# Kernel tuning notes

Measured on AMD Instinct MI355X. Metric: run time of the kernel, lower is better.

The kernel has to match this reference:

```python
import jax, jax.numpy as jnp
import numpy as np

NX = 65536      # x_steps_soil
T_STEPS = 200   # t_steps
HID = 32        # function_learner hidden width


def setup_inputs() -> dict:
    key = jax.random.key(0)
    ks = jax.random.split(key, 6)
    # u0: stacked (c, sk) initial state, values in [0, 1)
    u0 = jax.random.uniform(ks[0], (NX, 2), dtype=jnp.float32)
    t = jnp.arange(T_STEPS, dtype=jnp.float32)  # uniform time grid, dt = 1

    def lin(k, fan_in, fan_out):
        W = jax.random.normal(k, (fan_in, fan_out), dtype=jnp.float32) / np.float32(np.sqrt(fan_in))
        b = jnp.zeros((fan_out,), dtype=jnp.float32)
        return W, b

    # func_r: [1 -> 32 -> 32 -> 32 -> 1], tanh hidden, sigmoid output (sigmoid=True)
    W0, b0 = lin(ks[1], 1, HID)
    W1, b1 = lin(ks[2], HID, HID)
    W2, b2 = lin(ks[3], HID, HID)
    W3, b3 = lin(ks[4], HID, 1)

    return dict(
        u0=u0, t=t,
        W0=W0, b0=b0, W1=W1, b1=b1, W2=W2, b2=b2, W3=W3, b3=b3,
        ret_fac=jnp.float32(1.0),            # self.ret_fac
        D=jnp.float32(1e-5),                 # diffusion coefficient
        stencil=jnp.array([-1.0, 1.0], dtype=jnp.float32),
        BC=jnp.float32(1.0),                 # top Dirichlet BC value
        f=jnp.float32(0.5),                  # kinetic/instantaneous sorption share
        k_d=jnp.float32(1.0),                # Freundlich constant
        beta=jnp.float32(0.8),               # Freundlich exponent
        alpha=jnp.float32(0.05),             # kinetic rate constant
        rho_s=jnp.float32(1.5),              # bulk density
        n_e=jnp.float32(0.3),                # porosity
        v_e=jnp.float32(0.005),              # effective velocity
        dx=jnp.float32(0.01),                # spatial step
    )


def reference(u0, t, W0, b0, W1, b1, W2, b2, W3, b3,
              ret_fac, D, stencil, BC, f, k_d, beta, alpha, rho_s, n_e, v_e, dx):
    dt = t[1] - t[0]

    def mlp_r(c):
        # per-cell learned retardation multiplier (func_r), sigmoid output in (0,1)
        h = jnp.tanh(c[:, None] @ W0 + b0)   # [Nx, H]
        h = jnp.tanh(h @ W1 + b1)
        h = jnp.tanh(h @ W2 + b2)
        return jax.nn.sigmoid(h @ W3 + b3)[:, 0]  # [Nx]

    def rhs(u):
        c, sk = u[:, 0], u[:, 1]
        ret = mlp_r(c) * ret_fac
        # neighbor values: Dirichlet BC at top, zero-gradient at bottom
        cl = jnp.concatenate([jnp.full((1,), BC, dtype=c.dtype), c[:-1]])
        cr = jnp.concatenate([c[1:], c[-1:]])
        # stencil fluxes (stencil = [-1, 1])
        lf = stencil[0] * c + stencil[1] * cl
        lf = lf.at[0].multiply(2.0)  # half-cell distance at Dirichlet boundary
        rf = stencil[0] * c + stencil[1] * cr  # rf[-1] == 0: no-flux bottom
        diff = D / dx**2 * (lf + rf)
        # upwind advection (flow from top to bottom)
        adv = v_e / dx * (c - cl)
        # two-site sorption kinetics (Freundlich isotherm)
        dsk = alpha * ((1.0 - f) * k_d * jnp.power(jnp.clip(c, 1e-9, None), beta) - sk)
        dc = ret * (diff - adv) - (rho_s / n_e) * dsk
        return jnp.stack([dc, dsk], axis=-1)  # [Nx, 2]

    def step(u, _):
        u2 = u + dt * rhs(u)
        return u2, u2

    _, traj = jax.lax.scan(step, u0, None, length=t.shape[0])
    return traj  # [T, Nx, 2]
```

## Files before the change

kernel.cpp:

```cpp
#include <hip/hip_runtime.h>
#include <stdint.h>

#define NXS    65536
#define HID    32
#define BTL    512
#define NB     256
#define OWNB   256
#define MARG   200
#define SSPAN  656
#define SLAB   128
#define EPOCH  24
#define LUT_N  1024
#define NREP   16
#define LUT_SC   512.0f
#define LUT_BF   128.0f

typedef float    f32x4 __attribute__((ext_vector_type(4)));
typedef uint32_t u32x4 __attribute__((ext_vector_type(4)));

__device__ __forceinline__ float fexp2(float x) { return __builtin_amdgcn_exp2f(x); }
__device__ __forceinline__ float frcp(float x)  { return __builtin_amdgcn_rcpf(x); }
__device__ __forceinline__ float flog2(float x) { return __builtin_amdgcn_logf(x); }

__device__ __forceinline__ float dpp_up(float x) {
    int xi = __float_as_int(x);
    return __int_as_float(__builtin_amdgcn_update_dpp(xi, xi, 0x138, 0xF, 0xF, false));
}
__device__ __forceinline__ float dpp_down(float x) {
    int xi = __float_as_int(x);
    return __int_as_float(__builtin_amdgcn_update_dpp(xi, xi, 0x130, 0xF, 0xF, false));
}

__device__ __forceinline__ float fast_tanh(float x) {
    x = fminf(fmaxf(x, -15.0f), 15.0f);
    float e = fexp2(x * 2.8853900817779268f);
    return (e - 1.0f) * frcp(e + 1.0f);
}
__device__ __forceinline__ float fast_sigmoid(float x) {
    float e = fexp2(x * -1.4426950408889634f);
    return frcp(1.0f + e);
}

struct FinnPtrs {
    const float* tvec;
    const float* Dp;  const float* stencil; const float* BCp; const float* fp;
    const float* kdp; const float* betap;   const float* alphap; const float* rhosp;
    const float* nep; const float* vep;     const float* dxp;
};

__global__ __launch_bounds__(256) void finn_lut(
    const float* __restrict__ W0, const float* __restrict__ b0,
    const float* __restrict__ W1, const float* __restrict__ b1,
    const float* __restrict__ W2, const float* __restrict__ b2,
    const float* __restrict__ W3, const float* __restrict__ b3,
    const float* __restrict__ ret_fac, const float* __restrict__ betap,
    float2* __restrict__ rep)
{
    const int i = blockIdx.x * 256 + threadIdx.x;
    if (i >= LUT_N) return;
    const float c = -0.25f + ((float)i + 0.5f) * (1.0f / LUT_SC);

    float h[HID], a[HID];
    #pragma unroll
    for (int j = 0; j < HID; ++j)
        h[j] = fast_tanh(fmaf(c, W0[j], b0[j]));

    #pragma unroll
    for (int j = 0; j < HID; ++j) a[j] = b1[j];
    #pragma unroll
    for (int k = 0; k < HID; ++k) {
        const float hk = h[k];
        #pragma unroll
        for (int j = 0; j < HID; ++j) a[j] = fmaf(hk, W1[k * HID + j], a[j]);
    }
    #pragma unroll
    for (int j = 0; j < HID; ++j) h[j] = fast_tanh(a[j]);

    #pragma unroll
    for (int j = 0; j < HID; ++j) a[j] = b2[j];
    #pragma unroll
    for (int k = 0; k < HID; ++k) {
        const float hk = h[k];
        #pragma unroll
        for (int j = 0; j < HID; ++j) a[j] = fmaf(hk, W2[k * HID + j], a[j]);
    }
    #pragma unroll
    for (int j = 0; j < HID; ++j) h[j] = fast_tanh(a[j]);

    float pre = b3[0];
    #pragma unroll
    for (int k = 0; k < HID; ++k) pre = fmaf(h[k], W3[k], pre);

    const float ret = fast_sigmoid(pre) * ret_fac[0];
    const float pw  = fexp2(betap[0] * flog2(fmaxf(c, 1e-9f)));
    const float2 e = make_float2(ret, pw);
    #pragma unroll
    for (int r = 0; r < NREP; ++r)
        rep[i * NREP + r] = e;
}

__global__ __launch_bounds__(BTL, 2) void finn_sweep(
    const float* __restrict__ uin, float* __restrict__ out,
    const float2* __restrict__ rep_g, FinnPtrs P, int T, uint32_t outBytes)
{
    __shared__ float2 slut[LUT_N * NREP];
    __shared__ float2 xbuf[SSPAN];

    const int tid  = threadIdx.x;
    const int w    = tid >> 6;
    const int lane = tid & 63;
    const int r15  = lane & 15;

    {
        const f32x4* src4 = (const f32x4*)rep_g;
        f32x4* dst4 = (f32x4*)slut;
        #pragma unroll
        for (int j = 0; j < (LUT_N * NREP * 8 / 16) / BTL; ++j)
            dst4[tid + j * BTL] = src4[tid + j * BTL];
    }

    const float dt   = P.tvec[1] - P.tvec[0];
    const float s0   = P.stencil[0];
    const float s1   = P.stencil[1];
    const float dx   = P.dxp[0];
    const float A    = P.Dp[0] / (dx * dx);
    const float B    = P.vep[0] / dx;
    const float BC   = P.BCp[0];
    const float alp  = P.alphap[0];
    const float akd  = (1.0f - P.fp[0]) * P.kdp[0];
    const float rsne = P.rhosp[0] / P.nep[0];

    const float G     = dt * rsne * alp;
    const float mGAKD = -G * akd;
    const float S1c   = 1.0f - dt * alp;
    const float S2c   = dt * alp * akd;
    const float K1u   = dt * (2.0f * A * s0 - B);
    const float K2u   = dt * (A * s1 + B);
    const float K3u   = dt * A * s1;

    const int b = blockIdx.x;
    int blockBase = b * OWNB - MARG;
    if (blockBase < 0) blockBase = 0;
    if (blockBase > NXS - SSPAN) blockBase = NXS - SSPAN;
    const bool leftA  = (blockBase == 0);
    const bool rightA = (blockBase == NXS - SSPAN);
    const int ownRelL = b * OWNB - blockBase;
    const int ownRelR = ownRelL + OWNB;

    u32x4 srd;
    {
        const uint64_t op = (uint64_t)(uintptr_t)out;
        srd.x = (uint32_t)op;
        srd.y = (uint32_t)(op >> 32);
        srd.z = outBytes;
        srd.w = 0x00020000u;
    }

    int a = ((SSPAN - SLAB) * w / 7 + 1) & ~1;

    float c0, sk0, c1, sk1;
    {
        const f32x4* u4 = (const f32x4*)uin;
        const f32x4 u = u4[(blockBase + a + lane * 2) >> 1];
        c0 = u.x; sk0 = u.y; c1 = u.z; sk1 = u.w;
    }

    __syncthreads();

    int done = 0;
    while (done < T) {
        int nst = T - done; if (nst > EPOCH) nst = EPOCH;
        const int si = a + lane * 2;
        const int g0 = blockBase + si;

        float K0_0 = 0.0f, K1_0 = K1u, K2_0 = K2u;
        const float K3_0 = K3u;
        float K1_1 = K1u, K3_1 = K3u;
        const float K2_1 = K2u;
        if (g0 == 0)           { K0_0 = dt * BC * (2.0f * A * s1 + B);
                                 K1_0 = dt * (3.0f * A * s0 - B); K2_0 = 0.0f; }
        if (g0 + 1 == NXS - 1) { K1_1 = dt * (2.0f * A * s0 - B + A * s1);
                                 K3_1 = 0.0f; }

        const int vL = leftA ? 0 : done;
        const int vR = rightA ? SSPAN : SSPAN - done;
        const int pd = vR - vL - SLAB;
        const int aPrev = vL + ((pd * (w - 1) / 7 + 1) & ~1);
        const int aNext = vL + ((pd * (w + 1) / 7 + 1) & ~1);
        int bLo = (w == 0) ? 0     : (((aPrev + SLAB + a) >> 1) & ~1);
        int bHi = (w == 7) ? SSPAN : (((a + SLAB + aNext) >> 1) & ~1);
        if (bLo < ownRelL) bLo = ownRelL;
        if (bHi > ownRelR) bHi = ownRelR;
        const bool st = (si >= bLo) && (si < bHi);
        uint32_t voff = st ? (uint32_t)((done * NXS + g0) * 8) : 0x60000000u;

        float clS = dpp_up(c1);
        float crS = dpp_down(c0);
        int i0 = (int)__builtin_amdgcn_fmed3f(fmaf(c0, LUT_SC, LUT_BF), 0.0f, 1023.0f);
        int i1 = (int)__builtin_amdgcn_fmed3f(fmaf(c1, LUT_SC, LUT_BF), 0.0f, 1023.0f);
        float2 E0 = slut[(i0 << 4) | r15];
        float2 E1 = slut[(i1 << 4) | r15];

        for (int s = 0; s < nst; ++s) {
            float t0 = fmaf(K1_0, c0, K0_0);
            t0 = fmaf(K2_0, clS, t0);
            t0 = fmaf(K3_0, c1, t0);
            float t1 = K1_1 * c1;
            t1 = fmaf(K2_1, c0, t1);
            t1 = fmaf(K3_1, crS, t1);

            float v0 = fmaf(E0.x, t0, c0); v0 = fmaf(mGAKD, E0.y, v0);
            float v1 = fmaf(E1.x, t1, c1); v1 = fmaf(mGAKD, E1.y, v1);
            const float nc0 = fmaf(G, sk0, v0);
            const float nc1 = fmaf(G, sk1, v1);
            sk0 = fmaf(S1c, sk0, S2c * E0.y);
            sk1 = fmaf(S1c, sk1, S2c * E1.y);
            c0 = nc0; c1 = nc1;

            i0 = (int)__builtin_amdgcn_fmed3f(fmaf(c0, LUT_SC, LUT_BF), 0.0f, 1023.0f);
            i1 = (int)__builtin_amdgcn_fmed3f(fmaf(c1, LUT_SC, LUT_BF), 0.0f, 1023.0f);
            E0 = slut[(i0 << 4) | r15];
            E1 = slut[(i1 << 4) | r15];
            clS = dpp_up(c1);
            crS = dpp_down(c0);

            f32x4 ov; ov.x = c0; ov.y = sk0; ov.z = c1; ov.w = sk1;
            asm volatile("buffer_store_dwordx4 %0, %1, %2, 0 offen"
                         :: "v"(ov), "v"(voff), "s"(srd) : "memory");
            voff += (uint32_t)(NXS * 8);
        }

        done += nst;
        if (done >= T) break;

        asm volatile("s_waitcnt lgkmcnt(0)" ::: "memory");
        __builtin_amdgcn_s_barrier();
        asm volatile("" ::: "memory");
        {
            const int wLo = (w == 0 && leftA)  ? 0    : EPOCH;
            const int wHi = (w == 7 && rightA) ? SLAB : SLAB - EPOCH;
            const int sr = lane * 2;
            if (sr >= wLo && sr < wHi)         xbuf[a + sr]     = make_float2(c0, sk0);
            if (sr + 1 >= wLo && sr + 1 < wHi) xbuf[a + sr + 1] = make_float2(c1, sk1);
        }
        asm volatile("s_waitcnt lgkmcnt(0)" ::: "memory");
        __builtin_amdgcn_s_barrier();
        asm volatile("" ::: "memory");
        {
            const int vL2 = leftA ? 0 : done;
            const int vR2 = rightA ? SSPAN : SSPAN - done;
            const int pd2 = vR2 - vL2 - SLAB;
            a = vL2 + ((pd2 * w / 7 + 1) & ~1);
            const f32x4 u = *(const f32x4*)&xbuf[a + lane * 2];
            c0 = u.x; sk0 = u.y; c1 = u.z; sk1 = u.w;
        }
        asm volatile("s_waitcnt lgkmcnt(0)" ::: "memory");
        __builtin_amdgcn_s_barrier();
        asm volatile("" ::: "memory");
    }
}

extern "C" void kernel_launch(void* const* d_in, const int* in_sizes, int n_in,
                              void* d_out, int out_size, void* d_ws, size_t ws_size,
                              hipStream_t stream)
{
    const float* u0 = (const float*)d_in[0];
    FinnPtrs P;
    P.tvec    = (const float*)d_in[1];
    const float* W0      = (const float*)d_in[2];
    const float* b0      = (const float*)d_in[3];
    const float* W1      = (const float*)d_in[4];
    const float* b1      = (const float*)d_in[5];
    const float* W2      = (const float*)d_in[6];
    const float* b2      = (const float*)d_in[7];
    const float* W3      = (const float*)d_in[8];
    const float* b3      = (const float*)d_in[9];
    const float* ret_fac = (const float*)d_in[10];
    P.Dp      = (const float*)d_in[11];
    P.stencil = (const float*)d_in[12];
    P.BCp     = (const float*)d_in[13];
    P.fp      = (const float*)d_in[14];
    P.kdp     = (const float*)d_in[15];
    P.betap   = (const float*)d_in[16];
    P.alphap  = (const float*)d_in[17];
    P.rhosp   = (const float*)d_in[18];
    P.nep     = (const float*)d_in[19];
    P.vep     = (const float*)d_in[20];
    P.dxp     = (const float*)d_in[21];

    float*  out = (float*)d_out;
    float2* rep = (float2*)d_ws;
    const int T = in_sizes[1];

    hipLaunchKernelGGL(finn_lut, dim3(LUT_N / 256), dim3(256), 0, stream,
                       W0, b0, W1, b1, W2, b2, W3, b3, ret_fac, P.betap, rep);

    hipLaunchKernelGGL(finn_sweep, dim3(NB), dim3(BTL), 0, stream,
                       u0, out, rep, P, T, (uint32_t)out_size * 4u);
}
```

Baseline: 62.65 us.

## Fuse LUT build into sweep kernel with linear interpolation and software-pipelined lookups

Drops the separate LUT kernel. Each block now evaluates the MLP on 1024 grid points itself, and stores slope/intercept pairs so the retardation is linearly interpolated instead of piecewise-constant. The Freundlich power is computed exactly with exp2/log2 per step rather than read from the table. After a safe number of steps, the LDS lookup for the next step is issued ahead of the arithmetic to hide latency. The trade-off is that every block repeats the MLP work, and each step does more transcendental math.

```diff
diff --git a/kernel.cpp b/kernel.cpp
--- a/kernel.cpp
+++ b/kernel.cpp
@@ -10,10 +10,11 @@
 #define SSPAN  656
 #define SLAB   128
 #define EPOCH  24
+#define SAFE_T 48
 #define LUT_N  1024
 #define NREP   16
-#define LUT_SC   512.0f
-#define LUT_BF   128.0f
+#define LUT_SC 512.0f
+#define LUT_BF 128.0f
 
 typedef float    f32x4 __attribute__((ext_vector_type(4)));
 typedef uint32_t u32x4 __attribute__((ext_vector_type(4)));
@@ -41,6 +42,11 @@
     return frcp(1.0f + e);
 }
 
+struct FinnW {
+    const float* W0; const float* b0; const float* W1; const float* b1;
+    const float* W2; const float* b2; const float* W3; const float* b3;
+    const float* ret_fac;
+};
 struct FinnPtrs {
     const float* tvec;
     const float* Dp;  const float* stencil; const float* BCp; const float* fp;
@@ -48,60 +54,40 @@
     const float* nep; const float* vep;     const float* dxp;
 };
 
-__global__ __launch_bounds__(256) void finn_lut(
-    const float* __restrict__ W0, const float* __restrict__ b0,
-    const float* __restrict__ W1, const float* __restrict__ b1,
-    const float* __restrict__ W2, const float* __restrict__ b2,
-    const float* __restrict__ W3, const float* __restrict__ b3,
-    const float* __restrict__ ret_fac, const float* __restrict__ betap,
-    float2* __restrict__ rep)
-{
-    const int i = blockIdx.x * 256 + threadIdx.x;
-    if (i >= LUT_N) return;
-    const float c = -0.25f + ((float)i + 0.5f) * (1.0f / LUT_SC);
-
+__device__ float mlp_ret(float c, const FinnW& W) {
     float h[HID], a[HID];
     #pragma unroll
     for (int j = 0; j < HID; ++j)
-        h[j] = fast_tanh(fmaf(c, W0[j], b0[j]));
-
-    #pragma unroll
-    for (int j = 0; j < HID; ++j) a[j] = b1[j];
+        h[j] = fast_tanh(fmaf(c, W.W0[j], W.b0[j]));
+    #pragma unroll
+    for (int j = 0; j < HID; ++j) a[j] = W.b1[j];
     #pragma unroll
     for (int k = 0; k < HID; ++k) {
         const float hk = h[k];
         #pragma unroll
-        for (int j = 0; j < HID; ++j) a[j] = fmaf(hk, W1[k * HID + j], a[j]);
+        for (int j = 0; j < HID; ++j) a[j] = fmaf(hk, W.W1[k * HID + j], a[j]);
     }
     #pragma unroll
     for (int j = 0; j < HID; ++j) h[j] = fast_tanh(a[j]);
-
-    #pragma unroll
-    for (int j = 0; j < HID; ++j) a[j] = b2[j];
+    #pragma unroll
+    for (int j = 0; j < HID; ++j) a[j] = W.b2[j];
     #pragma unroll
     for (int k = 0; k < HID; ++k) {
         const float hk = h[k];
         #pragma unroll
-        for (int j = 0; j < HID; ++j) a[j] = fmaf(hk, W2[k * HID + j], a[j]);
+        for (int j = 0; j < HID; ++j) a[j] = fmaf(hk, W.W2[k * HID + j], a[j]);
     }
     #pragma unroll
     for (int j = 0; j < HID; ++j) h[j] = fast_tanh(a[j]);
-
-    float pre = b3[0];
-    #pragma unroll
-    for (int k = 0; k < HID; ++k) pre = fmaf(h[k], W3[k], pre);
-
-    const float ret = fast_sigmoid(pre) * ret_fac[0];
-    const float pw  = fexp2(betap[0] * flog2(fmaxf(c, 1e-9f)));
-    const float2 e = make_float2(ret, pw);
-    #pragma unroll
-    for (int r = 0; r < NREP; ++r)
-        rep[i * NREP + r] = e;
-}
-
-__global__ __launch_bounds__(BTL, 2) void finn_sweep(
+    float pre = W.b3[0];
+    #pragma unroll
+    for (int k = 0; k < HID; ++k) pre = fmaf(h[k], W.W3[k], pre);
+    return fast_sigmoid(pre) * W.ret_fac[0];
+}
+
+__global__ __launch_bounds__(BTL, 2) void finn_all(
     const float* __restrict__ uin, float* __restrict__ out,
-    const float2* __restrict__ rep_g, FinnPtrs P, int T, uint32_t outBytes)
+    FinnW W, FinnPtrs P, int T, uint32_t outBytes)
 {
     __shared__ float2 slut[LUT_N * NREP];
     __shared__ float2 xbuf[SSPAN];
@@ -111,12 +97,20 @@
     const int lane = tid & 63;
     const int r15  = lane & 15;
 
-    {
-        const f32x4* src4 = (const f32x4*)rep_g;
-        f32x4* dst4 = (f32x4*)slut;
+    float* raw = (float*)xbuf;
+    raw[tid]       = mlp_ret(-0.25f + (float)tid * (1.0f / LUT_SC), W);
+    raw[tid + 512] = mlp_ret(-0.25f + (float)(tid + 512) * (1.0f / LUT_SC), W);
+    __syncthreads();
+    #pragma unroll
+    for (int q = 0; q < 2; ++q) {
+        const int bin = tid + q * 512;
+        const float r0 = raw[bin];
+        const float r1 = (bin == LUT_N - 1) ? r0 : raw[bin + 1];
+        const float sl = (r1 - r0) * LUT_SC;
+        const float ic = fmaf(-(float)(bin - 128), r1 - r0, r0);
+        const float2 e = make_float2(sl, ic);
         #pragma unroll
-        for (int j = 0; j < (LUT_N * NREP * 8 / 16) / BTL; ++j)
-            dst4[tid + j * BTL] = src4[tid + j * BTL];
+        for (int r = 0; r < NREP; ++r) slut[(bin << 4) | r] = e;
     }
 
     const float dt   = P.tvec[1] - P.tvec[0];
@@ -126,6 +120,7 @@
     const float A    = P.Dp[0] / (dx * dx);
     const float B    = P.vep[0] / dx;
     const float BC   = P.BCp[0];
+    const float beta = P.betap[0];
     const float alp  = P.alphap[0];
     const float akd  = (1.0f - P.fp[0]) * P.kdp[0];
     const float rsne = P.rhosp[0] / P.nep[0];
@@ -201,33 +196,76 @@
         float2 E0 = slut[(i0 << 4) | r15];
         float2 E1 = slut[(i1 << 4) | r15];
 
-        for (int s = 0; s < nst; ++s) {
-            float t0 = fmaf(K1_0, c0, K0_0);
-            t0 = fmaf(K2_0, clS, t0);
-            t0 = fmaf(K3_0, c1, t0);
-            float t1 = K1_1 * c1;
-            t1 = fmaf(K2_1, c0, t1);
-            t1 = fmaf(K3_1, crS, t1);
-
-            float v0 = fmaf(E0.x, t0, c0); v0 = fmaf(mGAKD, E0.y, v0);
-            float v1 = fmaf(E1.x, t1, c1); v1 = fmaf(mGAKD, E1.y, v1);
-            const float nc0 = fmaf(G, sk0, v0);
-            const float nc1 = fmaf(G, sk1, v1);
-            sk0 = fmaf(S1c, sk0, S2c * E0.y);
-            sk1 = fmaf(S1c, sk1, S2c * E1.y);
-            c0 = nc0; c1 = nc1;
-
-            i0 = (int)__builtin_amdgcn_fmed3f(fmaf(c0, LUT_SC, LUT_BF), 0.0f, 1023.0f);
-            i1 = (int)__builtin_amdgcn_fmed3f(fmaf(c1, LUT_SC, LUT_BF), 0.0f, 1023.0f);
-            E0 = slut[(i0 << 4) | r15];
-            E1 = slut[(i1 << 4) | r15];
-            clS = dpp_up(c1);
-            crS = dpp_down(c0);
-
-            f32x4 ov; ov.x = c0; ov.y = sk0; ov.z = c1; ov.w = sk1;
-            asm volatile("buffer_store_dwordx4 %0, %1, %2, 0 offen"
-                         :: "v"(ov), "v"(voff), "s"(srd) : "memory");
-            voff += (uint32_t)(NXS * 8);
+        if (done < SAFE_T) {
+            for (int s = 0; s < nst; ++s) {
+                float t0 = fmaf(K1_0, c0, K0_0);
+                t0 = fmaf(K2_0, clS, t0);
+                t0 = fmaf(K3_0, c1, t0);
+                float t1 = K1_1 * c1;
+                t1 = fmaf(K2_1, c0, t1);
+                t1 = fmaf(K3_1, crS, t1);
+
+                const float ret0 = fmaf(c0, E0.x, E0.y);
+                const float ret1 = fmaf(c1, E1.x, E1.y);
+                const float pw0 = fexp2(beta * flog2(fmaxf(c0, 1e-9f)));
+                const float pw1 = fexp2(beta * flog2(fmaxf(c1, 1e-9f)));
+
+                float v0 = fmaf(ret0, t0, c0); v0 = fmaf(mGAKD, pw0, v0);
+                float v1 = fmaf(ret1, t1, c1); v1 = fmaf(mGAKD, pw1, v1);
+                const float nc0 = fmaf(G, sk0, v0);
+                const float nc1 = fmaf(G, sk1, v1);
+                sk0 = fmaf(S1c, sk0, S2c * pw0);
+                sk1 = fmaf(S1c, sk1, S2c * pw1);
+                c0 = nc0; c1 = nc1;
+
+                i0 = (int)__builtin_amdgcn_fmed3f(fmaf(c0, LUT_SC, LUT_BF), 0.0f, 1023.0f);
+                i1 = (int)__builtin_amdgcn_fmed3f(fmaf(c1, LUT_SC, LUT_BF), 0.0f, 1023.0f);
+                E0 = slut[(i0 << 4) | r15];
+                E1 = slut[(i1 << 4) | r15];
+                clS = dpp_up(c1);
+                crS = dpp_down(c0);
+
+                f32x4 ov; ov.x = c0; ov.y = sk0; ov.z = c1; ov.w = sk1;
+                asm volatile("buffer_store_dwordx4 %0, %1, %2, 0 offen"
+                             :: "v"(ov), "v"(voff), "s"(srd) : "memory");
+                voff += (uint32_t)(NXS * 8);
+            }
+        } else {
+            for (int s = 0; s < nst; ++s) {
+                const int n0 = (int)__builtin_amdgcn_fmed3f(fmaf(c0, LUT_SC, LUT_BF), 0.0f, 1023.0f);
+                const int n1 = (int)__builtin_amdgcn_fmed3f(fmaf(c1, LUT_SC, LUT_BF), 0.0f, 1023.0f);
+                const float2 EN0 = slut[(n0 << 4) | r15];
+                const float2 EN1 = slut[(n1 << 4) | r15];
+
+                float t0 = fmaf(K1_0, c0, K0_0);
+                t0 = fmaf(K2_0, clS, t0);
+                t0 = fmaf(K3_0, c1, t0);
+                float t1 = K1_1 * c1;
+                t1 = fmaf(K2_1, c0, t1);
+                t1 = fmaf(K3_1, crS, t1);
+
+                const float ret0 = fmaf(c0, E0.x, E0.y);
+                const float ret1 = fmaf(c1, E1.x, E1.y);
+                const float pw0 = fexp2(beta * flog2(fmaxf(c0, 1e-9f)));
+                const float pw1 = fexp2(beta * flog2(fmaxf(c1, 1e-9f)));
+
+                float v0 = fmaf(ret0, t0, c0); v0 = fmaf(mGAKD, pw0, v0);
+                float v1 = fmaf(ret1, t1, c1); v1 = fmaf(mGAKD, pw1, v1);
+                const float nc0 = fmaf(G, sk0, v0);
+                const float nc1 = fmaf(G, sk1, v1);
+                sk0 = fmaf(S1c, sk0, S2c * pw0);
+                sk1 = fmaf(S1c, sk1, S2c * pw1);
+                c0 = nc0; c1 = nc1;
+
+                clS = dpp_up(c1);
+                crS = dpp_down(c0);
+                E0 = EN0; E1 = EN1;
+
+                f32x4 ov; ov.x = c0; ov.y = sk0; ov.z = c1; ov.w = sk1;
+                asm volatile("buffer_store_dwordx4 %0, %1, %2, 0 offen"
+                             :: "v"(ov), "v"(voff), "s"(srd) : "memory");
+                voff += (uint32_t)(NXS * 8);
+            }
         }
 
         done += nst;
@@ -265,17 +303,18 @@
                               hipStream_t stream)
 {
     const float* u0 = (const float*)d_in[0];
+    FinnW W;
     FinnPtrs P;
     P.tvec    = (const float*)d_in[1];
-    const float* W0      = (const float*)d_in[2];
-    const float* b0      = (const float*)d_in[3];
-    const float* W1      = (const float*)d_in[4];
-    const float* b1      = (const float*)d_in[5];
-    const float* W2      = (const float*)d_in[6];
-    const float* b2      = (const float*)d_in[7];
-    const float* W3      = (const float*)d_in[8];
-    const float* b3      = (const float*)d_in[9];
-    const float* ret_fac = (const float*)d_in[10];
+    W.W0      = (const float*)d_in[2];
+    W.b0      = (const float*)d_in[3];
+    W.W1      = (const float*)d_in[4];
+    W.b1      = (const float*)d_in[5];
+    W.W2      = (const float*)d_in[6];
+    W.b2      = (const float*)d_in[7];
+    W.W3      = (const float*)d_in[8];
+    W.b3      = (const float*)d_in[9];
+    W.ret_fac = (const float*)d_in[10];
     P.Dp      = (const float*)d_in[11];
     P.stencil = (const float*)d_in[12];
     P.BCp     = (const float*)d_in[13];
@@ -288,13 +327,9 @@
     P.vep     = (const float*)d_in[20];
     P.dxp     = (const float*)d_in[21];
 
-    float*  out = (float*)d_out;
-    float2* rep = (float2*)d_ws;
+    float* out  = (float*)d_out;
     const int T = in_sizes[1];
 
-    hipLaunchKernelGGL(finn_lut, dim3(LUT_N / 256), dim3(256), 0, stream,
-                       W0, b0, W1, b1, W2, b2, W3, b3, ret_fac, P.betap, rep);
-
-    hipLaunchKernelGGL(finn_sweep, dim3(NB), dim3(BTL), 0, stream,
-                       u0, out, rep, P, T, (uint32_t)out_size * 4u);
-}
+    hipLaunchKernelGGL(finn_all, dim3(NB), dim3(BTL), 0, stream,
+                       u0, out, W, P, T, (uint32_t)out_size * 4u);
+}
```

Result: slower. 84.25 us (+34.5%).
